# Performance work log

Measured on AMD Instinct MI355X. Metric: run time of the kernel, lower is better.

Reference implementation:

```python
import jax, jax.numpy as jnp
import numpy as np

B, T, D, H = 4, 4096, 2048, 128  # head_size = embedding_size // num_heads = 2048 // 16

def setup_inputs() -> dict:
    key = jax.random.key(0)
    kx, kq, kk, kv = jax.random.split(key, 4)
    x = jax.random.normal(kx, (B, T, D), dtype=jnp.float32)
    # Dense kernels with normal(0.01) init as in the module
    Wq = 0.01 * jax.random.normal(kq, (D, H), dtype=jnp.float32)
    Wk = 0.01 * jax.random.normal(kk, (D, H), dtype=jnp.float32)
    Wv = 0.01 * jax.random.normal(kv, (D, H), dtype=jnp.float32)
    return {"x": x, "Wq": Wq, "Wk": Wk, "Wv": Wv}

def reference(x, Wq, Wk, Wv):
    # Q/K/V projections: Dense(features=head_size, use_bias=False)
    Q = jnp.einsum('BTD,DH->BTH', x, Wq)
    K = jnp.einsum('BTD,DH->BTH', x, Wk)
    V = jnp.einsum('BTD,DH->BTH', x, Wv)
    scale = 1.0 / jnp.sqrt(jnp.asarray(K.shape[-1], dtype=x.dtype))
    scores = jnp.einsum('BTH,BSH->BTS', Q, K) * scale  # (B, T, T)
    weights = jax.nn.softmax(scores, axis=-1)
    # dropout rate 0.0 (deterministic) -> identity
    out = jnp.einsum('BTS,BSH->BTH', weights, V)  # (B, T, H)
    return out
```

## Files before the change

kernel.cpp:

```cpp
#include <hip/hip_runtime.h>
#include <hip/hip_bf16.h>
#include <math.h>

#define B_ 4
#define T_ 4096
#define D_ 2048
#define H_ 128
#define M_ (B_*T_)

typedef __bf16 bf16;
typedef __attribute__((ext_vector_type(8))) __bf16 bf16x8;
typedef __attribute__((ext_vector_type(4))) float f32x4;
typedef __attribute__((ext_vector_type(16))) float f32x16;

#define MFMA32(a,b,c) __builtin_amdgcn_mfma_f32_32x32x16_bf16(a,b,c,0,0,0)

typedef __attribute__((address_space(3))) unsigned int lds_u32_t;
typedef const __attribute__((address_space(1))) unsigned int glb_u32_t;

__device__ __forceinline__ void cp16(void* lds, const void* g) {
    __builtin_amdgcn_global_load_lds((glb_u32_t*)g, (lds_u32_t*)lds, 16, 0, 0);
}

#define QOFF   0u
#define KOFF   (4u<<20)
#define VTOFF  (8u<<20)
#define WTOFF  (12u<<20)
#define OPOFF  (14u<<20)
#define LPOFF  (OPOFF + 8388608u)

__global__ __launch_bounds__(256) void cvtw_kernel(
    const float* __restrict__ Wq, const float* __restrict__ Wk,
    const float* __restrict__ Wv, bf16* __restrict__ Wtb)
{
    __shared__ __align__(16) bf16 U[128 * 72];
    const int tid = threadIdx.x;
    const int m  = blockIdx.x >> 5;
    const int kt = blockIdx.x & 31;
    const int k0 = kt * 64;
    const float* W = (m == 0) ? Wq : ((m == 1) ? Wk : Wv);
    const float sc = (m == 0) ? 0.12753102105128444f : 1.0f;

    #pragma unroll
    for (int u = 0; u < 8; u++) {
        int id = tid + u * 256;
        int kr = id >> 5, c4 = id & 31;
        float4 v = *(const float4*)(W + (size_t)(k0 + kr) * H_ + c4 * 4);
        U[(c4*4 + 0) * 72 + kr] = (bf16)(v.x * sc);
        U[(c4*4 + 1) * 72 + kr] = (bf16)(v.y * sc);
        U[(c4*4 + 2) * 72 + kr] = (bf16)(v.z * sc);
        U[(c4*4 + 3) * 72 + kr] = (bf16)(v.w * sc);
    }
    __syncthreads();
    #pragma unroll
    for (int u = 0; u < 4; u++) {
        int id = tid + u * 256;
        int n = id >> 3, kc = id & 7;
        bf16x8 v = *(const bf16x8*)((const char*)U + n * 144 + kc * 16);
        *(bf16x8*)((char*)Wtb + (size_t)m * 524288 + (size_t)n * 4096
                   + k0 * 2 + kc * 16) = v;
    }
}

__global__ __launch_bounds__(512, 2) void proj_kernel(
    const float* __restrict__ X, const bf16* __restrict__ Wtb,
    bf16* __restrict__ Qb, bf16* __restrict__ Kb, bf16* __restrict__ Vtb)
{
    __shared__ __align__(16) char smem[114688];

    const int tid = threadIdx.x;
    const int w = tid >> 6, lane = tid & 63;
    const int c31 = lane & 31, kh = lane >> 5;
    const int mh = w >> 2;
    const int ng = w & 3;
    const int m0 = blockIdx.x * 64;

    f32x16 acc[3];
    #pragma unroll
    for (int t = 0; t < 3; t++)
        #pragma unroll
        for (int r = 0; r < 16; r++) acc[t][r] = 0.f;

    #pragma unroll
    for (int u = 0; u < 6; u++) {
        int s = tid + u * 512;
        int n = s >> 3, ccs = s & 7;
        int kc = ccs ^ (n & 7);
        int mat = n >> 7, ncol = n & 127;
        cp16(smem + 16384 + s * 16,
             (const char*)Wtb + (size_t)mat * 524288 + (size_t)ncol * 4096 + kc * 16);
    }
    {
        int r = tid >> 3, cc = tid & 7;
        const float* src = X + (size_t)(m0 + r) * D_ + cc * 8;
        float4 v0 = *(const float4*)src;
        float4 v1 = *(const float4*)(src + 4);
        union { bf16 h[8]; uint4 u4; } pk;
        pk.h[0]=(bf16)v0.x; pk.h[1]=(bf16)v0.y; pk.h[2]=(bf16)v0.z; pk.h[3]=(bf16)v0.w;
        pk.h[4]=(bf16)v1.x; pk.h[5]=(bf16)v1.y; pk.h[6]=(bf16)v1.z; pk.h[7]=(bf16)v1.w;
        *(uint4*)(smem + (r * 8 + (cc ^ (r & 7))) * 16) = pk.u4;
    }
    __syncthreads();

    for (int it = 0; it < 32; it++) {
        const int cur = it & 1;
        char* xcur = smem + cur * 8192;
        char* wcur = smem + 16384 + cur * 49152;
        float4 xv0, xv1;
        if (it < 31) {
            const int k1 = (it + 1) * 64;
            char* wnxt = smem + 16384 + (cur ^ 1) * 49152;
            #pragma unroll
            for (int u = 0; u < 6; u++) {
                int s = tid + u * 512;
                int n = s >> 3, ccs = s & 7;
                int kc = ccs ^ (n & 7);
                int mat = n >> 7, ncol = n & 127;
                cp16(wnxt + s * 16,
                     (const char*)Wtb + (size_t)mat * 524288 + (size_t)ncol * 4096
                     + k1 * 2 + kc * 16);
            }
            int r = tid >> 3, cc = tid & 7;
            const float* src = X + (size_t)(m0 + r) * D_ + k1 + cc * 8;
            xv0 = *(const float4*)src;
            xv1 = *(const float4*)(src + 4);
        }
        #pragma unroll
        for (int s = 0; s < 4; s++) {
            int c = s * 2 + kh;
            int rr = mh * 32 + c31;
            bf16x8 af = *(const bf16x8*)(xcur + (rr * 8 + (c ^ (rr & 7))) * 16);
            #pragma unroll
            for (int t = 0; t < 3; t++) {
                int n = ng * 96 + t * 32 + c31;
                bf16x8 bfr = *(const bf16x8*)(wcur + (n * 8 + (c ^ (n & 7))) * 16);
                acc[t] = MFMA32(af, bfr, acc[t]);
            }
        }
        if (it < 31) {
            char* xnxt = smem + (cur ^ 1) * 8192;
            int r = tid >> 3, cc = tid & 7;
            union { bf16 h[8]; uint4 u4; } pk;
            pk.h[0]=(bf16)xv0.x; pk.h[1]=(bf16)xv0.y; pk.h[2]=(bf16)xv0.z; pk.h[3]=(bf16)xv0.w;
            pk.h[4]=(bf16)xv1.x; pk.h[5]=(bf16)xv1.y; pk.h[6]=(bf16)xv1.z; pk.h[7]=(bf16)xv1.w;
            *(uint4*)(xnxt + (r * 8 + (cc ^ (r & 7))) * 16) = pk.u4;
        }
        __syncthreads();
    }

    #pragma unroll
    for (int t = 0; t < 3; t++) {
        int nb = ng * 96 + t * 32;
        if ((nb >> 7) == 2) {
            int ncol = (nb & 127) + c31;
            #pragma unroll
            for (int g = 0; g < 4; g++) {
                int m = m0 + mh * 32 + g * 8 + kh * 4;
                union { bf16 h[4]; uint2 u2; } pk;
                #pragma unroll
                for (int e = 0; e < 4; e++) pk.h[e] = (bf16)acc[t][g*4 + e];
                *(uint2*)((char*)Vtb + (size_t)ncol * 32768 + (size_t)m * 2) = pk.u2;
            }
        }
    }
    bf16* U = (bf16*)smem;
    #pragma unroll
    for (int mat = 0; mat < 2; mat++) {
        __syncthreads();
        #pragma unroll
        for (int t = 0; t < 3; t++) {
            int nb = ng * 96 + t * 32;
            if ((nb >> 7) == mat) {
                int lcol = (nb & 127) + c31;
                #pragma unroll
                for (int r = 0; r < 16; r++) {
                    int row = mh * 32 + (r & 3) + 8 * (r >> 2) + 4 * kh;
                    U[row * 136 + lcol] = (bf16)acc[t][r];
                }
            }
        }
        __syncthreads();
        bf16* og = (mat == 0) ? Qb : Kb;
        #pragma unroll
        for (int u = 0; u < 2; u++) {
            int id = tid + u * 512;
            int rr = id >> 4, cc = id & 15;
            bf16x8 v = *(const bf16x8*)((const char*)U + rr * 272 + cc * 16);
            *(bf16x8*)((char*)og + (size_t)(m0 + rr) * 256 + cc * 16) = v;
        }
    }
}

__global__ __launch_bounds__(256, 2) void attn_kernel(
    const bf16* __restrict__ Qb, const bf16* __restrict__ Kb,
    const bf16* __restrict__ Vtb,
    float* __restrict__ Out0, float* __restrict__ Opart1,
    float* __restrict__ lpart)
{
    __shared__ __align__(16) char smem[75264];

    const int tid = threadIdx.x;
    const int w = tid >> 6, lane = tid & 63;
    const int c31 = lane & 31, kh = lane >> 5;

    const int bx = blockIdx.x;
    const int slice = bx & 7;
    const int qt = bx >> 3;
    const int b  = slice >> 1;
    const int ks = slice & 1;
    const int row0 = b*T_ + qt*64;
    const int kvrow = b*T_ + ks*2048;

    const int mh  = w >> 1;
    const int kh2 = w & 1;
    const int nq0 = (w & 1) * 2;

    bf16x8 qf[8];
    {
        const char* qrow = (const char*)Qb + (size_t)(row0 + mh*32 + c31)*256 + kh*16;
        #pragma unroll
        for (int s = 0; s < 8; s++)
            qf[s] = *(const bf16x8*)(qrow + s*32);
    }

    f32x16 o0, o1;
    #pragma unroll
    for (int r = 0; r < 16; r++) { o0[r] = 0.f; o1[r] = 0.f; }
    float lsum[16];
    #pragma unroll
    for (int r = 0; r < 16; r++) lsum[r] = 0.f;

    #pragma unroll
    for (int u = 0; u < 4; u++) {
        int s = tid + u*256;
        int r = s >> 4, csw = s & 15;
        int cg = (csw & 8) | ((csw ^ r) & 7);
        cp16(smem + s*16, (const char*)Kb + (size_t)(kvrow + r)*256 + cg*16);
    }
    #pragma unroll
    for (int u = 0; u < 4; u++) {
        int s = tid + u*256;
        int h = s >> 3, ccsw = s & 7;
        int cc = (ccsw ^ h) & 7;
        cp16(smem + 32768 + s*16,
             (const char*)Vtb + (size_t)h*32768 + (size_t)kvrow*2 + cc*16);
    }
    __syncthreads();

    for (int it = 0; it < 32; it++) {
        const int cur = it & 1;
        char* ksb = smem + cur*16384;
        char* vsb = smem + 32768 + cur*16384;
        if (it < 31) {
            const int knx = kvrow + (it + 1)*64;
            char* kn = smem + (cur ^ 1)*16384;
            char* vn = smem + 32768 + (cur ^ 1)*16384;
            #pragma unroll
            for (int u = 0; u < 4; u++) {
                int s = tid + u*256;
                int r = s >> 4, csw = s & 15;
                int cg = (csw & 8) | ((csw ^ r) & 7);
                cp16(kn + s*16, (const char*)Kb + (size_t)(knx + r)*256 + cg*16);
            }
            #pragma unroll
            for (int u = 0; u < 4; u++) {
                int s = tid + u*256;
                int h = s >> 3, ccsw = s & 7;
                int cc = (ccsw ^ h) & 7;
                cp16(vn + s*16,
                     (const char*)Vtb + (size_t)h*32768 + (size_t)knx*2 + cc*16);
            }
        }

        f32x16 sacc;
        #pragma unroll
        for (int r = 0; r < 16; r++) sacc[r] = 0.f;
        const int key = kh2*32 + c31;
        #pragma unroll
        for (int s = 0; s < 8; s++) {
            int ck = s*2 + kh;
            int slot = key*16 + ((ck & 8) | ((ck ^ key) & 7));
            bf16x8 kf = *(const bf16x8*)(ksb + slot*16);
            sacc = MFMA32(qf[s], kf, sacc);
        }
        bf16* Pp = (bf16*)(smem + 65536);
        #pragma unroll
        for (int r = 0; r < 16; r++) {
            float p = exp2f(sacc[r]);
            lsum[r] += p;
            int irow = (r & 3) + 8*(r >> 2) + 4*kh;
            Pp[(mh*32 + irow)*72 + key] = (bf16)p;
        }
        __syncthreads();

        #pragma unroll
        for (int s2 = 0; s2 < 4; s2++) {
            bf16x8 pf = *(const bf16x8*)(smem + 65536
                           + (mh*32 + c31)*144 + s2*32 + kh*16);
            int cv = s2*2 + kh;
            int n0 = nq0*32 + c31;
            int n1 = n0 + 32;
            bf16x8 vf0 = *(const bf16x8*)(vsb + (n0*8 + ((cv ^ n0) & 7))*16);
            bf16x8 vf1 = *(const bf16x8*)(vsb + (n1*8 + ((cv ^ n1) & 7))*16);
            o0 = MFMA32(pf, vf0, o0);
            o1 = MFMA32(pf, vf1, o1);
        }
        __syncthreads();
    }

    #pragma unroll
    for (int r = 0; r < 16; r++) {
        float v = lsum[r];
        v += __shfl_xor(v, 1); v += __shfl_xor(v, 2); v += __shfl_xor(v, 4);
        v += __shfl_xor(v, 8); v += __shfl_xor(v, 16);
        if (c31 == 0) {
            int irow = (r & 3) + 8*(r >> 2) + 4*kh;
            ((float*)(smem + 74752))[kh2*64 + mh*32 + irow] = v;
        }
    }
    __syncthreads();
    if (tid < 64) {
        const float* lr = (const float*)(smem + 74752);
        lpart[ks*M_ + row0 + tid] = lr[tid] + lr[64 + tid];
    }
    float* Od = (ks == 0) ? Out0 : Opart1;
    #pragma unroll
    for (int r = 0; r < 16; r++) {
        int m = mh*32 + (r & 3) + 8*(r >> 2) + 4*kh;
        Od[(size_t)(row0 + m)*H_ + nq0*32 + c31] = o0[r];
        Od[(size_t)(row0 + m)*H_ + nq0*32 + 32 + c31] = o1[r];
    }
}

__global__ __launch_bounds__(256) void merge_kernel(
    float* __restrict__ Out, const float* __restrict__ Op1,
    const float* __restrict__ lp)
{
    int id = blockIdx.x * 256 + threadIdx.x;
    int row = id >> 5;
    float inv = 1.0f / (lp[row] + lp[M_ + row]);
    float4 a = *(const float4*)(Out + (size_t)id*4);
    float4 bq = *(const float4*)(Op1 + (size_t)id*4);
    float4 rr;
    rr.x = (a.x + bq.x) * inv; rr.y = (a.y + bq.y) * inv;
    rr.z = (a.z + bq.z) * inv; rr.w = (a.w + bq.w) * inv;
    *(float4*)(Out + (size_t)id*4) = rr;
}

extern "C" void kernel_launch(void* const* d_in, const int* in_sizes, int n_in,
                              void* d_out, int out_size, void* d_ws, size_t ws_size,
                              hipStream_t stream) {
    const float* x  = (const float*)d_in[0];
    const float* Wq = (const float*)d_in[1];
    const float* Wk = (const float*)d_in[2];
    const float* Wv = (const float*)d_in[3];
    float* outp = (float*)d_out;
    char* ws = (char*)d_ws;

    bf16* Qb  = (bf16*)(ws + QOFF);
    bf16* Kb  = (bf16*)(ws + KOFF);
    bf16* Vtb = (bf16*)(ws + VTOFF);
    bf16* Wtb = (bf16*)(ws + WTOFF);
    float* Op1 = (float*)(ws + OPOFF);
    float* lp  = (float*)(ws + LPOFF);

    cvtw_kernel<<<96, 256, 0, stream>>>(Wq, Wk, Wv, Wtb);
    proj_kernel<<<M_/64, 512, 0, stream>>>(x, Wtb, Qb, Kb, Vtb);
    attn_kernel<<<512, 256, 0, stream>>>(Qb, Kb, Vtb, outp, Op1, lp);
    merge_kernel<<<2048, 256, 0, stream>>>(outp, Op1, lp);
}
```

Measured before the change: 276.8 us.

## Enlarge attention query tile to 128 rows and split keys four ways

The attention kernel now processes 128 query rows per block instead of 64, with the key range split into four slices of 1024 instead of two of 2048. The score MMA moves to 16x16x32 MFMA with a transposed K-by-Q operand order. V becomes single-buffered and is prefetched after the PV stage, which frees LDS. Each K/V tile loaded into LDS is now reused by twice as many query rows, cutting LDS and global traffic per FLOP, at the cost of more partial outputs for the merge kernel to read and reduce.

```diff
diff --git a/kernel.cpp b/kernel.cpp
--- a/kernel.cpp
+++ b/kernel.cpp
@@ -13,6 +13,7 @@
 typedef __attribute__((ext_vector_type(4))) float f32x4;
 typedef __attribute__((ext_vector_type(16))) float f32x16;
 
+#define MFMA16(a,b,c) __builtin_amdgcn_mfma_f32_16x16x32_bf16(a,b,c,0,0,0)
 #define MFMA32(a,b,c) __builtin_amdgcn_mfma_f32_32x32x16_bf16(a,b,c,0,0,0)
 
 typedef __attribute__((address_space(3))) unsigned int lds_u32_t;
@@ -27,7 +28,7 @@
 #define VTOFF  (8u<<20)
 #define WTOFF  (12u<<20)
 #define OPOFF  (14u<<20)
-#define LPOFF  (OPOFF + 8388608u)
+#define LPOFF  (OPOFF + 25165824u)
 
 __global__ __launch_bounds__(256) void cvtw_kernel(
     const float* __restrict__ Wq, const float* __restrict__ Wk,
@@ -194,41 +195,45 @@
 __global__ __launch_bounds__(256, 2) void attn_kernel(
     const bf16* __restrict__ Qb, const bf16* __restrict__ Kb,
     const bf16* __restrict__ Vtb,
-    float* __restrict__ Out0, float* __restrict__ Opart1,
+    float* __restrict__ Out0, float* __restrict__ Opart,
     float* __restrict__ lpart)
 {
-    __shared__ __align__(16) char smem[75264];
+    __shared__ __align__(16) char smem[68608];
 
     const int tid = threadIdx.x;
     const int w = tid >> 6, lane = tid & 63;
+    const int c15 = lane & 15, quad = (lane >> 4) & 3;
     const int c31 = lane & 31, kh = lane >> 5;
 
     const int bx = blockIdx.x;
-    const int slice = bx & 7;
-    const int qt = bx >> 3;
-    const int b  = slice >> 1;
-    const int ks = slice & 1;
-    const int row0 = b*T_ + qt*64;
-    const int kvrow = b*T_ + ks*2048;
-
-    const int mh  = w >> 1;
-    const int kh2 = w & 1;
-    const int nq0 = (w & 1) * 2;
-
-    bf16x8 qf[8];
-    {
-        const char* qrow = (const char*)Qb + (size_t)(row0 + mh*32 + c31)*256 + kh*16;
-        #pragma unroll
-        for (int s = 0; s < 8; s++)
-            qf[s] = *(const bf16x8*)(qrow + s*32);
-    }
-
-    f32x16 o0, o1;
-    #pragma unroll
-    for (int r = 0; r < 16; r++) { o0[r] = 0.f; o1[r] = 0.f; }
-    float lsum[16];
-    #pragma unroll
-    for (int r = 0; r < 16; r++) lsum[r] = 0.f;
+    const int slice = bx & 15;
+    const int qt = bx >> 4;
+    const int b = slice >> 2, ks = slice & 3;
+    const int row0 = b*T_ + qt*128;
+    const int kvrow = b*T_ + ks*1024;
+
+    const int kg = w & 1;
+    const int ms = w >> 1;
+    const int nh = w & 1;
+
+    bf16x8 qf[4][4];
+    #pragma unroll
+    for (int mg = 0; mg < 4; mg++) {
+        const char* qrow = (const char*)Qb
+            + (size_t)(row0 + ms*64 + mg*16 + c15) * 256 + quad*16;
+        #pragma unroll
+        for (int kk = 0; kk < 4; kk++)
+            qf[mg][kk] = *(const bf16x8*)(qrow + kk*64);
+    }
+
+    f32x16 o[2][2];
+    #pragma unroll
+    for (int g = 0; g < 2; g++)
+        #pragma unroll
+        for (int nn = 0; nn < 2; nn++)
+            #pragma unroll
+            for (int r = 0; r < 16; r++) o[g][nn][r] = 0.f;
+    float lsum[4] = {0.f, 0.f, 0.f, 0.f};
 
     #pragma unroll
     for (int u = 0; u < 4; u++) {
@@ -247,14 +252,12 @@
     }
     __syncthreads();
 
-    for (int it = 0; it < 32; it++) {
+    for (int it = 0; it < 16; it++) {
         const int cur = it & 1;
         char* ksb = smem + cur*16384;
-        char* vsb = smem + 32768 + cur*16384;
-        if (it < 31) {
+        if (it < 15) {
             const int knx = kvrow + (it + 1)*64;
             char* kn = smem + (cur ^ 1)*16384;
-            char* vn = smem + 32768 + (cur ^ 1)*16384;
             #pragma unroll
             for (int u = 0; u < 4; u++) {
                 int s = tid + u*256;
@@ -262,88 +265,116 @@
                 int cg = (csw & 8) | ((csw ^ r) & 7);
                 cp16(kn + s*16, (const char*)Kb + (size_t)(knx + r)*256 + cg*16);
             }
+        }
+
+        bf16* Pp = (bf16*)(smem + 49152);
+        #pragma unroll
+        for (int kg16 = 0; kg16 < 2; kg16++) {
+            const int key = kg*32 + kg16*16 + c15;
+            bf16x8 kf[4];
+            #pragma unroll
+            for (int kk = 0; kk < 4; kk++) {
+                int ck = kk*4 + quad;
+                kf[kk] = *(const bf16x8*)(ksb
+                           + (key*16 + ((ck & 8) | ((ck ^ key) & 7)))*16);
+            }
+            #pragma unroll
+            for (int mg = 0; mg < 4; mg++) {
+                f32x4 sc = (f32x4){0.f,0.f,0.f,0.f};
+                #pragma unroll
+                for (int kk = 0; kk < 4; kk++)
+                    sc = MFMA16(kf[kk], qf[mg][kk], sc);
+                int m = ms*64 + mg*16 + c15;
+                int k0 = kg*32 + kg16*16 + quad*4;
+                union { bf16 h[4]; uint2 u2; } pk;
+                #pragma unroll
+                for (int r = 0; r < 4; r++) {
+                    float p = exp2f(sc[r]);
+                    lsum[mg] += p;
+                    pk.h[r] = (bf16)p;
+                }
+                *(uint2*)((char*)Pp + m*144 + k0*2) = pk.u2;
+            }
+        }
+        __syncthreads();
+
+        char* vsb = smem + 32768;
+        #pragma unroll
+        for (int s2 = 0; s2 < 4; s2++) {
+            int cv = s2*2 + kh;
+            bf16x8 pf[2], vfr[2];
+            #pragma unroll
+            for (int g = 0; g < 2; g++)
+                pf[g] = *(const bf16x8*)(smem + 49152
+                           + (ms*64 + g*32 + c31)*144 + s2*32 + kh*16);
+            #pragma unroll
+            for (int nn = 0; nn < 2; nn++) {
+                int n = nh*64 + nn*32 + c31;
+                vfr[nn] = *(const bf16x8*)(vsb + (n*8 + ((cv ^ n) & 7))*16);
+            }
+            #pragma unroll
+            for (int g = 0; g < 2; g++)
+                #pragma unroll
+                for (int nn = 0; nn < 2; nn++)
+                    o[g][nn] = MFMA32(pf[g], vfr[nn], o[g][nn]);
+        }
+        __syncthreads();
+
+        if (it < 15) {
+            const int knx = kvrow + (it + 1)*64;
             #pragma unroll
             for (int u = 0; u < 4; u++) {
                 int s = tid + u*256;
                 int h = s >> 3, ccsw = s & 7;
                 int cc = (ccsw ^ h) & 7;
-                cp16(vn + s*16,
+                cp16(smem + 32768 + s*16,
                      (const char*)Vtb + (size_t)h*32768 + (size_t)knx*2 + cc*16);
             }
         }
-
-        f32x16 sacc;
-        #pragma unroll
-        for (int r = 0; r < 16; r++) sacc[r] = 0.f;
-        const int key = kh2*32 + c31;
-        #pragma unroll
-        for (int s = 0; s < 8; s++) {
-            int ck = s*2 + kh;
-            int slot = key*16 + ((ck & 8) | ((ck ^ key) & 7));
-            bf16x8 kf = *(const bf16x8*)(ksb + slot*16);
-            sacc = MFMA32(qf[s], kf, sacc);
-        }
-        bf16* Pp = (bf16*)(smem + 65536);
-        #pragma unroll
-        for (int r = 0; r < 16; r++) {
-            float p = exp2f(sacc[r]);
-            lsum[r] += p;
-            int irow = (r & 3) + 8*(r >> 2) + 4*kh;
-            Pp[(mh*32 + irow)*72 + key] = (bf16)p;
-        }
-        __syncthreads();
-
-        #pragma unroll
-        for (int s2 = 0; s2 < 4; s2++) {
-            bf16x8 pf = *(const bf16x8*)(smem + 65536
-                           + (mh*32 + c31)*144 + s2*32 + kh*16);
-            int cv = s2*2 + kh;
-            int n0 = nq0*32 + c31;
-            int n1 = n0 + 32;
-            bf16x8 vf0 = *(const bf16x8*)(vsb + (n0*8 + ((cv ^ n0) & 7))*16);
-            bf16x8 vf1 = *(const bf16x8*)(vsb + (n1*8 + ((cv ^ n1) & 7))*16);
-            o0 = MFMA32(pf, vf0, o0);
-            o1 = MFMA32(pf, vf1, o1);
-        }
-        __syncthreads();
-    }
-
-    #pragma unroll
-    for (int r = 0; r < 16; r++) {
-        float v = lsum[r];
-        v += __shfl_xor(v, 1); v += __shfl_xor(v, 2); v += __shfl_xor(v, 4);
-        v += __shfl_xor(v, 8); v += __shfl_xor(v, 16);
-        if (c31 == 0) {
-            int irow = (r & 3) + 8*(r >> 2) + 4*kh;
-            ((float*)(smem + 74752))[kh2*64 + mh*32 + irow] = v;
-        }
+    }
+
+    float* lred = (float*)(smem + 67584);
+    #pragma unroll
+    for (int mg = 0; mg < 4; mg++) {
+        float v = lsum[mg];
+        v += __shfl_xor(v, 16);
+        v += __shfl_xor(v, 32);
+        if (lane < 16)
+            lred[kg*128 + ms*64 + mg*16 + c15] = v;
     }
     __syncthreads();
-    if (tid < 64) {
-        const float* lr = (const float*)(smem + 74752);
-        lpart[ks*M_ + row0 + tid] = lr[tid] + lr[64 + tid];
-    }
-    float* Od = (ks == 0) ? Out0 : Opart1;
-    #pragma unroll
-    for (int r = 0; r < 16; r++) {
-        int m = mh*32 + (r & 3) + 8*(r >> 2) + 4*kh;
-        Od[(size_t)(row0 + m)*H_ + nq0*32 + c31] = o0[r];
-        Od[(size_t)(row0 + m)*H_ + nq0*32 + 32 + c31] = o1[r];
-    }
+    if (tid < 128)
+        lpart[ks*M_ + row0 + tid] = lred[tid] + lred[128 + tid];
+
+    float* Od = (ks == 0) ? Out0 : (Opart + (size_t)(ks - 1) * M_ * H_);
+    #pragma unroll
+    for (int g = 0; g < 2; g++)
+        #pragma unroll
+        for (int nn = 0; nn < 2; nn++)
+            #pragma unroll
+            for (int r = 0; r < 16; r++) {
+                int m = ms*64 + g*32 + (r & 3) + 8*(r >> 2) + 4*kh;
+                int n = nh*64 + nn*32 + c31;
+                Od[(size_t)(row0 + m)*H_ + n] = o[g][nn][r];
+            }
 }
 
 __global__ __launch_bounds__(256) void merge_kernel(
-    float* __restrict__ Out, const float* __restrict__ Op1,
+    float* __restrict__ Out, const float* __restrict__ Opart,
     const float* __restrict__ lp)
 {
     int id = blockIdx.x * 256 + threadIdx.x;
     int row = id >> 5;
-    float inv = 1.0f / (lp[row] + lp[M_ + row]);
+    float inv = 1.0f / (lp[row] + lp[M_ + row] + lp[2*M_ + row] + lp[3*M_ + row]);
     float4 a = *(const float4*)(Out + (size_t)id*4);
-    float4 bq = *(const float4*)(Op1 + (size_t)id*4);
+    float4 b1 = *(const float4*)(Opart + (size_t)id*4);
+    float4 b2 = *(const float4*)(Opart + (size_t)M_*H_ + (size_t)id*4);
+    float4 b3 = *(const float4*)(Opart + (size_t)2*M_*H_ + (size_t)id*4);
     float4 rr;
-    rr.x = (a.x + bq.x) * inv; rr.y = (a.y + bq.y) * inv;
-    rr.z = (a.z + bq.z) * inv; rr.w = (a.w + bq.w) * inv;
+    rr.x = (a.x + b1.x + b2.x + b3.x) * inv;
+    rr.y = (a.y + b1.y + b2.y + b3.y) * inv;
+    rr.z = (a.z + b1.z + b2.z + b3.z) * inv;
+    rr.w = (a.w + b1.w + b2.w + b3.w) * inv;
     *(float4*)(Out + (size_t)id*4) = rr;
 }
 
@@ -361,11 +392,11 @@
     bf16* Kb  = (bf16*)(ws + KOFF);
     bf16* Vtb = (bf16*)(ws + VTOFF);
     bf16* Wtb = (bf16*)(ws + WTOFF);
-    float* Op1 = (float*)(ws + OPOFF);
+    float* Op  = (float*)(ws + OPOFF);
     float* lp  = (float*)(ws + LPOFF);
 
     cvtw_kernel<<<96, 256, 0, stream>>>(Wq, Wk, Wv, Wtb);
     proj_kernel<<<M_/64, 512, 0, stream>>>(x, Wtb, Qb, Kb, Vtb);
-    attn_kernel<<<512, 256, 0, stream>>>(Qb, Kb, Vtb, outp, Op1, lp);
-    merge_kernel<<<2048, 256, 0, stream>>>(outp, Op1, lp);
-}
+    attn_kernel<<<512, 256, 0, stream>>>(Qb, Kb, Vtb, outp, Op, lp);
+    merge_kernel<<<2048, 256, 0, stream>>>(outp, Op, lp);
+}
```

Result: faster. 266.8 us (-3.6%).
